# Kernel optimization log

Hardware: AMD Instinct MI355X
Metric: run time of the kernel (lower is better)

## Reference

```python
import jax, jax.numpy as jnp
import numpy as np

TOP_K = 2
N_EXP = 64
EVAL_CAPACITY = 2.0


def setup_inputs() -> dict:
    key = jax.random.key(0)
    k1, k2 = jax.random.split(key)
    x = jax.random.normal(k1, (4, 4096, 2048), dtype=jnp.float32)
    w_g = jax.random.normal(k2, (N_EXP, 2048), dtype=jnp.float32) * 0.02  # Linear(n_embd, n_exp, bias=False)
    return {"x": x, "w_g": w_g}


def reference(x, w_g):
    B, T, C = x.shape
    num_tokens = B * T
    x_flat = x.reshape(num_tokens, C)
    # gating logits: [N, E]
    logits = jnp.einsum('nc,ec->ne', x_flat, w_g)
    # top-k selection
    top_k_logits, top_k_indices = jax.lax.top_k(logits, TOP_K)  # [N, k]
    router_probs = jax.nn.softmax(top_k_logits, axis=-1)        # [N, k]
    # static expert capacity (eval path)
    exp_capacity = max(int(TOP_K * EVAL_CAPACITY * num_tokens / N_EXP), 4)
    # one-hot expert mask [N, k, E]
    expert_mask = jax.nn.one_hot(top_k_indices, N_EXP, dtype=jnp.int32)
    # rank tokens within each expert via cumsum over (k-major, token) order
    reshaped = expert_mask.transpose(1, 0, 2).reshape(TOP_K * num_tokens, N_EXP)
    cumsum = jnp.cumsum(reshaped, axis=0)
    position = cumsum.reshape(TOP_K, num_tokens, N_EXP).transpose(1, 0, 2)  # [N, k, E]
    rank = (position - 1) * expert_mask
    capacity_mask = (rank < exp_capacity).astype(jnp.int32)
    final_mask = expert_mask * capacity_mask                     # [N, k, E]
    probs_mask = (final_mask.sum(axis=-1) > 0)                   # [N, k] bool
    router_probs_masked = router_probs * probs_mask.astype(router_probs.dtype)
    final_rank = rank.sum(axis=-1)                               # [N, k]
    return final_mask, router_probs_masked, top_k_indices, final_rank, exp_capacity
```

## Files before the change

kernel.cpp:

```cpp
#include <hip/hip_runtime.h>
#include <math.h>

#define C_DIM 2048
#define E_DIM 64
#define BT    32
#define NW    4

typedef _Float16 v8hf  __attribute__((ext_vector_type(8)));
typedef float    f32x4 __attribute__((ext_vector_type(4)));

#define SCALE      64.0f
#define INV_SCALE2 (1.0f/4096.0f)

typedef __attribute__((address_space(3))) char lds_char;

__device__ __forceinline__ void gl16(const void* g, lds_char* l)
{
    __builtin_amdgcn_global_load_lds((const __attribute__((address_space(1))) void*)g,
                                     (__attribute__((address_space(3))) void*)l, 16, 0, 0);
}

__launch_bounds__(256)
__global__ void k_wsplit(const float* __restrict__ w, _Float16* __restrict__ wfrag)
{
    int t  = blockIdx.x * 256 + threadIdx.x;
    int l  = t & 63;
    int ni = (t >> 6) & 3;
    int q  = t >> 8;
    int e  = 16 * ni + (l & 15);
    int k0 = 32 * q + (l >> 4) * 8;
    const float* src = w + (size_t)e * C_DIM + k0;
    float4 a = *(const float4*)(src);
    float4 b = *(const float4*)(src + 4);
    float s[8] = {a.x, a.y, a.z, a.w, b.x, b.y, b.z, b.w};
    v8hf hv, lv;
#pragma unroll
    for (int j = 0; j < 8; ++j) {
        float sc = s[j] * SCALE;
        _Float16 h = (_Float16)sc;
        hv[j] = h;
        lv[j] = (_Float16)(sc - (float)h);
    }
    size_t fo = (size_t)(q * 4 + ni) * 1024;
    *(v8hf*)(wfrag + fo + l * 8)       = hv;
    *(v8hf*)(wfrag + fo + 512 + l * 8) = lv;
}

__launch_bounds__(256, 2)
__global__ void k_logits_top2(const float* __restrict__ x, const _Float16* __restrict__ wfrag,
                              unsigned char* __restrict__ idx0, unsigned char* __restrict__ idx1,
                              float* __restrict__ dlt, unsigned short* __restrict__ gcounts,
                              int nblk)
{
    __shared__ alignas(16) char smem[65536];

    const int tid  = threadIdx.x;
    const int lane = tid & 63;
    const int wk   = tid >> 6;
    const int ln15 = lane & 15;
    const int g4   = lane >> 4;
    const int t0   = blockIdx.x * BT;

    f32x4 acc[2][4];
#pragma unroll
    for (int mi = 0; mi < 2; ++mi)
#pragma unroll
        for (int ni = 0; ni < 4; ++ni) acc[mi][ni] = (f32x4)0.0f;

    v8hf bh[2][4], bl[2][4];
    v8hf ah[2], al[2];

    const float* xlane = x + (size_t)(t0 + ln15) * C_DIM + 32 * wk + 8 * g4;
    const char*  wlane = (const char*)wfrag + (lane << 4);
    lds_char* s3    = (lds_char*)smem;
    lds_char* sbase = s3 + wk * 4096;

#define ISSUE_X(cc)                                                             \
    do {                                                                        \
        lds_char*    d  = sbase + (((cc) & 3) * 16384);                         \
        const float* gp = xlane + (cc) * 128;                                   \
        gl16(gp,                  d);                                           \
        gl16(gp + 4,              d + 1024);                                    \
        gl16(gp + 16 * C_DIM,     d + 2048);                                    \
        gl16(gp + 16 * C_DIM + 4, d + 3072);                                    \
    } while (0)

#define ISSUE_B(cc, s)                                                          \
    do {                                                                        \
        const char* wp = wlane + ((size_t)(4 * (cc) + wk) << 13);               \
        bh[s][0] = *(const v8hf*)(wp);          bl[s][0] = *(const v8hf*)(wp + 1024); \
        bh[s][1] = *(const v8hf*)(wp + 2048);   bl[s][1] = *(const v8hf*)(wp + 3072); \
        bh[s][2] = *(const v8hf*)(wp + 4096);   bl[s][2] = *(const v8hf*)(wp + 5120); \
        bh[s][3] = *(const v8hf*)(wp + 6144);   bl[s][3] = *(const v8hf*)(wp + 7168); \
    } while (0)

#define CVT(mi, lo, hi)                                                         \
    do {                                                                        \
        _Pragma("unroll")                                                       \
        for (int j = 0; j < 4; ++j) {                                           \
            float sc0 = (lo)[j] * SCALE;                                        \
            _Float16 h0 = (_Float16)sc0;                                        \
            ah[mi][j] = h0; al[mi][j] = (_Float16)(sc0 - (float)h0);            \
            float sc1 = (hi)[j] * SCALE;                                        \
            _Float16 h1 = (_Float16)sc1;                                        \
            ah[mi][j + 4] = h1; al[mi][j + 4] = (_Float16)(sc1 - (float)h1);    \
        }                                                                       \
    } while (0)

#define COMPUTE(cc, s)                                                          \
    do {                                                                        \
        const char* rb = smem + wk * 4096 + (((cc) & 3) * 16384) + lane * 16;   \
        f32x4 lo0 = *(const f32x4*)(rb);                                        \
        f32x4 hi0 = *(const f32x4*)(rb + 1024);                                 \
        f32x4 lo1 = *(const f32x4*)(rb + 2048);                                 \
        f32x4 hi1 = *(const f32x4*)(rb + 3072);                                 \
        CVT(0, lo0, hi0);                                                       \
        CVT(1, lo1, hi1);                                                       \
        _Pragma("unroll")                                                       \
        for (int ni = 0; ni < 4; ++ni) {                                        \
            acc[0][ni] = __builtin_amdgcn_mfma_f32_16x16x32_f16(ah[0], bh[s][ni], acc[0][ni], 0, 0, 0); \
            acc[0][ni] = __builtin_amdgcn_mfma_f32_16x16x32_f16(ah[0], bl[s][ni], acc[0][ni], 0, 0, 0); \
            acc[0][ni] = __builtin_amdgcn_mfma_f32_16x16x32_f16(al[0], bh[s][ni], acc[0][ni], 0, 0, 0); \
            acc[1][ni] = __builtin_amdgcn_mfma_f32_16x16x32_f16(ah[1], bh[s][ni], acc[1][ni], 0, 0, 0); \
            acc[1][ni] = __builtin_amdgcn_mfma_f32_16x16x32_f16(ah[1], bl[s][ni], acc[1][ni], 0, 0, 0); \
            acc[1][ni] = __builtin_amdgcn_mfma_f32_16x16x32_f16(al[1], bh[s][ni], acc[1][ni], 0, 0, 0); \
        }                                                                       \
    } while (0)

#define CHUNK(c, S)                                                             \
    asm volatile("s_waitcnt vmcnt(16)" ::: "memory");                           \
    COMPUTE(c, S);                                                              \
    ISSUE_B(((c) + 2) & 15, S);                                                 \
    ISSUE_X(((c) + 3) & 15);

    ISSUE_B(0, 0);
    ISSUE_X(0); ISSUE_X(1);
    ISSUE_B(1, 1);
    ISSUE_X(2);

    CHUNK(0, 0)  CHUNK(1, 1)  CHUNK(2, 0)  CHUNK(3, 1)
    CHUNK(4, 0)  CHUNK(5, 1)  CHUNK(6, 0)  CHUNK(7, 1)
    CHUNK(8, 0)  CHUNK(9, 1)  CHUNK(10, 0) CHUNK(11, 1)
    CHUNK(12, 0) CHUNK(13, 1) CHUNK(14, 0) CHUNK(15, 1)

    asm volatile("s_waitcnt vmcnt(0)" ::: "memory");
    __syncthreads();

    float* lgs = (float*)smem;
    int*   cnt = (int*)(smem + 8192);
    if (tid < 128) cnt[tid] = 0;
#pragma unroll
    for (int w = 0; w < NW; ++w) {
        if (w > 0) __syncthreads();
        if (wk == w) {
#pragma unroll
            for (int mi = 0; mi < 2; ++mi)
#pragma unroll
                for (int ni = 0; ni < 4; ++ni)
#pragma unroll
                    for (int gg = 0; gg < 4; ++gg) {
                        int row = 16 * mi + (g4 << 2) + gg;
                        int e   = 16 * ni + ln15;
                        float vv = acc[mi][ni][gg] * INV_SCALE2;
                        if (w == 0) lgs[row * 64 + e]  = vv;
                        else        lgs[row * 64 + e] += vv;
                    }
        }
    }
    __syncthreads();

#pragma unroll
    for (int t = 0; t < 8; ++t) {
        int rowl = (wk << 3) + t;
        float v = lgs[rowl * 64 + lane];
        float vv = v; int ix = lane;
#pragma unroll
        for (int off = 32; off > 0; off >>= 1) {
            float ov = __shfl_down(vv, off, 64);
            int   oi = __shfl_down(ix, off, 64);
            if (ov > vv || (ov == vv && oi < ix)) { vv = ov; ix = oi; }
        }
        int   i1 = __shfl(ix, 0, 64);
        float v1 = __shfl(vv, 0, 64);

        vv = (lane == i1) ? -3.0e38f : v; ix = lane;
#pragma unroll
        for (int off = 32; off > 0; off >>= 1) {
            float ov = __shfl_down(vv, off, 64);
            int   oi = __shfl_down(ix, off, 64);
            if (ov > vv || (ov == vv && oi < ix)) { vv = ov; ix = oi; }
        }
        int   i2 = __shfl(ix, 0, 64);
        float v2 = __shfl(vv, 0, 64);

        if (lane == 0) {
            int n = t0 + rowl;
            idx0[n] = (unsigned char)i1;
            idx1[n] = (unsigned char)i2;
            dlt[n]  = v2 - v1;
            atomicAdd(&cnt[i1], 1);
            atomicAdd(&cnt[64 + i2], 1);
        }
    }

    __syncthreads();
    if (tid < 128) {
        int e = tid & 63, k = tid >> 6;
        gcounts[(size_t)e * (2 * nblk) + k * nblk + blockIdx.x] = (unsigned short)cnt[tid];
    }
}

__launch_bounds__(64)
__global__ void k_scan2(unsigned short* __restrict__ g, int S)
{
    const int e = blockIdx.x, lane = threadIdx.x;
    unsigned short* row = g + (size_t)e * S;
    int vals[16];
    const int R = S >> 6;
#pragma unroll
    for (int r = 0; r < 16; ++r) if (r < R) vals[r] = row[(r << 6) + lane];
    int running = 0;
#pragma unroll
    for (int r = 0; r < 16; ++r) {
        if (r >= R) break;
        int v = vals[r], s = v;
#pragma unroll
        for (int off = 1; off < 64; off <<= 1) {
            int t = __shfl_up(s, off, 64);
            if (lane >= off) s += t;
        }
        row[(r << 6) + lane] = (unsigned short)(s - v + running);
        running += __shfl(s, 63, 64);
    }
}

__launch_bounds__(128)
__global__ void k_rank_out(const unsigned char* __restrict__ idx0, const unsigned char* __restrict__ idx1,
                           const unsigned short* __restrict__ gpre, const float* __restrict__ dlt,
                           float* __restrict__ out, int N, int cap, int nblk)
{
    const int b = blockIdx.x, tid = threadIdx.x;
    const int lane = tid & 63, kk = tid >> 6;
    const int t0 = b * BT;
    __shared__ int sm_ix[2][BT], sm_rk[2][BT];

    int v = -1, base = 0;
    if (lane < BT) {
        v = (kk ? idx1 : idx0)[t0 + lane];
        base = gpre[(size_t)v * (2 * nblk) + kk * nblk + b];
    }
    const unsigned long long ltm = (1ull << lane) - 1ull;
    int pre = 0;
    for (int e = 0; e < 64; ++e) {
        unsigned long long bb = __ballot(v == e);
        if (v == e) pre = __popcll(bb & ltm);
    }
    if (lane < BT) { sm_ix[kk][lane] = v; sm_rk[kk][lane] = base + pre; }
    __syncthreads();

#pragma unroll
    for (int rep = 0; rep < 8; ++rep) {
        int f   = tid + 128 * rep;
        int n2  = f >> 5;
        int rem = (f & 31) * 4;
        int kq  = rem >> 6;
        int e0  = rem & 63;
        int ix  = sm_ix[kq][n2];
        int rr  = sm_rk[kq][n2];
        float val = (rr < cap) ? 1.0f : 0.0f;
        float4 o = make_float4(0.f, 0.f, 0.f, 0.f);
        int d = ix - e0;
        if (d >= 0 && d < 4) ((float*)&o)[d] = val;
        *(float4*)(out + (size_t)(t0 + n2) * 128 + rem) = o;
    }

    size_t B = (size_t)2 * N * E_DIM;
    if (tid < 2 * BT) {
        int n2 = tid >> 1, kq = tid & 1;
        int n  = t0 + n2;
        int gi = 2 * n + kq;
        int ix = sm_ix[kq][n2];
        int rr = sm_rk[kq][n2];
        float d  = dlt[n];
        float e1 = expf(d);
        float inv = 1.0f / (1.0f + e1);
        float p  = kq ? (e1 * inv) : inv;
        bool keep = rr < cap;
        out[B + gi]         = keep ? p : 0.0f;
        out[B + 2 * N + gi] = (float)ix;
        out[B + 4 * N + gi] = (float)rr;
    }
    if (b == 0 && tid == 0) out[B + 6 * N] = (float)cap;
}

extern "C" void kernel_launch(void* const* d_in, const int* in_sizes, int n_in,
                              void* d_out, int out_size, void* d_ws, size_t ws_size,
                              hipStream_t stream)
{
    const float* x  = (const float*)d_in[0];
    const float* wg = (const float*)d_in[1];
    const int N = in_sizes[0] / C_DIM;
    const int nblk = N / BT;

    char* ws = (char*)d_ws;
    unsigned char*  idx0    = (unsigned char*)ws;
    unsigned char*  idx1    = idx0 + N;
    float*          dlt     = (float*)(idx1 + N);
    unsigned short* gcounts = (unsigned short*)(dlt + N);
    _Float16*       wfrag   = (_Float16*)(gcounts + (size_t)64 * 2 * nblk);

    float* out = (float*)d_out;

    int cap = (int)((long long)2 * 2 * N / E_DIM);
    if (cap < 4) cap = 4;

    k_wsplit<<<64, 256, 0, stream>>>(wg, wfrag);
    k_logits_top2<<<nblk, 256, 0, stream>>>(x, wfrag, idx0, idx1, dlt, gcounts, nblk);
    k_scan2<<<E_DIM, 64, 0, stream>>>(gcounts, 2 * nblk);
    k_rank_out<<<nblk, 128, 0, stream>>>(idx0, idx1, gcounts, dlt, out, N, cap, nblk);
}
```

Measured before the change: 234.5 us.

## Place scratch buffers inside output mask region and write mask in separate pass

Moves all intermediate scratch buffers (indices, deltas, per-block counts, fp16 weight fragments) from the workspace into the tail of the output mask region. The dense one-hot mask write is split out of the rank kernel into a new kernel that runs afterwards and overwrites that scratch space. It reads the already-written index and rank outputs to build the mask. The likely intent is better cache locality or working around workspace handling. The cost is one extra launch, a dependence on exact byte offsets and problem size, and a second read of the index and rank outputs.

```diff
diff --git a/kernel.cpp b/kernel.cpp
--- a/kernel.cpp
+++ b/kernel.cpp
@@ -235,9 +235,9 @@
 }
 
 __launch_bounds__(128)
-__global__ void k_rank_out(const unsigned char* __restrict__ idx0, const unsigned char* __restrict__ idx1,
-                           const unsigned short* __restrict__ gpre, const float* __restrict__ dlt,
-                           float* __restrict__ out, int N, int cap, int nblk)
+__global__ void k_rank_tail(const unsigned char* __restrict__ idx0, const unsigned char* __restrict__ idx1,
+                            const unsigned short* __restrict__ gpre, const float* __restrict__ dlt,
+                            float* __restrict__ out, int N, int cap, int nblk)
 {
     const int b = blockIdx.x, tid = threadIdx.x;
     const int lane = tid & 63, kk = tid >> 6;
@@ -257,22 +257,6 @@
     }
     if (lane < BT) { sm_ix[kk][lane] = v; sm_rk[kk][lane] = base + pre; }
     __syncthreads();
-
-#pragma unroll
-    for (int rep = 0; rep < 8; ++rep) {
-        int f   = tid + 128 * rep;
-        int n2  = f >> 5;
-        int rem = (f & 31) * 4;
-        int kq  = rem >> 6;
-        int e0  = rem & 63;
-        int ix  = sm_ix[kq][n2];
-        int rr  = sm_rk[kq][n2];
-        float val = (rr < cap) ? 1.0f : 0.0f;
-        float4 o = make_float4(0.f, 0.f, 0.f, 0.f);
-        int d = ix - e0;
-        if (d >= 0 && d < 4) ((float*)&o)[d] = val;
-        *(float4*)(out + (size_t)(t0 + n2) * 128 + rem) = o;
-    }
 
     size_t B = (size_t)2 * N * E_DIM;
     if (tid < 2 * BT) {
@@ -293,6 +277,25 @@
     if (b == 0 && tid == 0) out[B + 6 * N] = (float)cap;
 }
 
+__launch_bounds__(256)
+__global__ void k_mask(const float* __restrict__ tix, const float* __restrict__ trk,
+                       float* __restrict__ mask, int cap)
+{
+    int f = blockIdx.x * 256 + threadIdx.x;
+    int n   = f >> 5;
+    int rem = (f & 31) * 4;
+    int kq  = rem >> 6;
+    int e0  = rem & 63;
+    int gi  = 2 * n + kq;
+    int ix  = (int)tix[gi];
+    int rr  = (int)trk[gi];
+    float val = (rr < cap) ? 1.0f : 0.0f;
+    float4 o = make_float4(0.f, 0.f, 0.f, 0.f);
+    int d = ix - e0;
+    if (d >= 0 && d < 4) ((float*)&o)[d] = val;
+    ((float4*)mask)[f] = o;
+}
+
 extern "C" void kernel_launch(void* const* d_in, const int* in_sizes, int n_in,
                               void* d_out, int out_size, void* d_ws, size_t ws_size,
                               hipStream_t stream)
@@ -302,12 +305,20 @@
     const int N = in_sizes[0] / C_DIM;
     const int nblk = N / BT;
 
-    char* ws = (char*)d_ws;
-    unsigned char*  idx0    = (unsigned char*)ws;
-    unsigned char*  idx1    = idx0 + N;
-    float*          dlt     = (float*)(idx1 + N);
-    unsigned short* gcounts = (unsigned short*)(dlt + N);
-    _Float16*       wfrag   = (_Float16*)(gcounts + (size_t)64 * 2 * nblk);
+    (void)d_ws; (void)ws_size;
+    char* ob = (char*)d_out;
+    const size_t maskBytes  = (size_t)2 * N * E_DIM * 4;
+    const size_t wfragOff   = maskBytes - 524288;
+    const size_t gcountsOff = wfragOff - 131072;
+    const size_t dltOff     = gcountsOff - 65536;
+    const size_t idx1Off    = dltOff - 16384;
+    const size_t idx0Off    = idx1Off - 16384;
+
+    unsigned char*  idx0    = (unsigned char*)(ob + idx0Off);
+    unsigned char*  idx1    = (unsigned char*)(ob + idx1Off);
+    float*          dlt     = (float*)(ob + dltOff);
+    unsigned short* gcounts = (unsigned short*)(ob + gcountsOff);
+    _Float16*       wfrag   = (_Float16*)(ob + wfragOff);
 
     float* out = (float*)d_out;
 
@@ -317,5 +328,8 @@
     k_wsplit<<<64, 256, 0, stream>>>(wg, wfrag);
     k_logits_top2<<<nblk, 256, 0, stream>>>(x, wfrag, idx0, idx1, dlt, gcounts, nblk);
     k_scan2<<<E_DIM, 64, 0, stream>>>(gcounts, 2 * nblk);
-    k_rank_out<<<nblk, 128, 0, stream>>>(idx0, idx1, gcounts, dlt, out, N, cap, nblk);
-}
+    k_rank_tail<<<nblk, 128, 0, stream>>>(idx0, idx1, gcounts, dlt, out, N, cap, nblk);
+    k_mask<<<(N * 32) / 256, 256, 0, stream>>>(out + (size_t)2 * N * E_DIM + 2 * N,
+                                               out + (size_t)2 * N * E_DIM + 4 * N,
+                                               out, cap);
+}
```

New measurement: 237.4 us. Within noise of the previous version (+1.2%).
